# Optimization experiments

Measured on AMD Instinct MI355X. Metric: run time of the kernel, lower is better.

The kernel has to match this reference:

```python
import jax, jax.numpy as jnp
import numpy as np

# dims: N batch, L seq, H heads, d projection_dim, P position_dimension
N, Lq, Lk, H, d, P = 2, 1024, 1024, 8, 64, 1
D = H * d


def _kernel(x):
    # _log_exp_kernel: positive feature map log(1+exp(x)) (softplus)
    return jax.nn.softplus(x)


def setup_inputs() -> dict:
    key = jax.random.key(0)
    ks = jax.random.split(key, 8)
    sc = 1.0 / np.sqrt(D).astype(np.float32)
    return {
        "query": jax.random.normal(ks[0], (N, Lq, D), jnp.float32),
        "key_seq": jax.random.normal(ks[1], (N, Lk, D), jnp.float32),
        "Wq": jax.random.normal(ks[2], (D, D), jnp.float32) * sc,
        "Wk": jax.random.normal(ks[3], (D, D), jnp.float32) * sc,
        "Wv": jax.random.normal(ks[4], (D, D), jnp.float32) * sc,
        "position_coeffs": jax.random.uniform(ks[5], (H, d), jnp.float32, 0.5, 1.5),
        "position_weight": jax.random.normal(ks[6], (H, d, P), jnp.float32) * 1e-3,
        "position_bias": jax.random.normal(ks[7], (H, d), jnp.float32) * 1e-2,
    }


def reference(query, key_seq, Wq, Wk, Wv, position_coeffs, position_weight, position_bias):
    # torch Linear (no bias): y = x @ W.T
    q = _kernel(jnp.einsum('nld,ed->nle', query, Wq).reshape(N, Lq, H, d))
    k = _kernel(jnp.einsum('nld,ed->nle', key_seq, Wk).reshape(N, Lk, H, d))
    v = jnp.einsum('nld,ed->nle', key_seq, Wv).reshape(N, Lk, H, d)
    # (N, H, L, d)
    q = jnp.transpose(q, (0, 2, 1, 3))
    k = jnp.transpose(k, (0, 2, 1, 3))
    v = jnp.transpose(v, (0, 2, 1, 3))

    # default positions: arange, query_offset = 0
    qpos = jnp.broadcast_to(jnp.arange(Lq, dtype=jnp.float32).reshape(1, Lq, 1), (N, Lq, P))
    kpos = jnp.broadcast_to(jnp.arange(Lk, dtype=jnp.float32).reshape(1, Lk, 1), (N, Lk, P))
    pq = jnp.einsum('nlp,hkp->nhlk', qpos, position_weight) + position_bias[None, :, None, :]
    pk = jnp.einsum('nlp,hkp->nhlk', kpos, position_weight)

    coeff = position_coeffs[None, :, None, :]  # (1, H, 1, d)

    def part(f, values):
        # causal (mask_future) linear attention via inclusive cumsum over keys
        Qf = q * f(pq) * coeff           # (N, H, Lq, d)
        Kf = k * f(pk)                   # (N, H, Lk, d)
        S = jnp.cumsum(jnp.einsum('nhkd,nhke->nhkde', Kf, values), axis=2)
        return jnp.einsum('nhqd,nhqde->nhqe', Qf, S)

    num = part(jnp.cos, v) + part(jnp.sin, v)           # (N, H, Lq, d)
    unit = jnp.ones((N, H, Lk, 1), jnp.float32)
    den = part(jnp.cos, unit) + part(jnp.sin, unit)     # (N, H, Lq, 1)
    attn = num / den
    return jnp.transpose(attn, (0, 2, 1, 3)).reshape(N, Lq, D)
```

## Files before the change

kernel.cpp:

```cpp
#include <hip/hip_runtime.h>
#include <cmath>

#define NB    2
#define LSEQ  1024
#define NH    8
#define HD    64
#define DD    512
#define FDIM  128
#define EV    65
#define CHUNK 64
#define NC    16
#define NBH   16

typedef short short8 __attribute__((ext_vector_type(8)));
typedef float floatx4 __attribute__((ext_vector_type(4)));

__device__ __forceinline__ float softplusf(float x) {
  return fmaxf(x, 0.0f) + log1pf(expf(-fabsf(x)));
}

__device__ __forceinline__ unsigned short f2bf(float f) {
  unsigned u = __float_as_uint(f);
  u += 0x7fffu + ((u >> 16) & 1u);
  return (unsigned short)(u >> 16);
}

__device__ __forceinline__ short8 cvt8(float4 a, float4 b) {
  short8 r;
  r[0] = (short)f2bf(a.x); r[1] = (short)f2bf(a.y);
  r[2] = (short)f2bf(a.z); r[3] = (short)f2bf(a.w);
  r[4] = (short)f2bf(b.x); r[5] = (short)f2bf(b.y);
  r[6] = (short)f2bf(b.z); r[7] = (short)f2bf(b.w);
  return r;
}

__global__ __launch_bounds__(256) void k_proj(
    const float* __restrict__ Xq, const float* __restrict__ Xkv,
    const float* __restrict__ Wq, const float* __restrict__ Wk,
    const float* __restrict__ Wv, const float* __restrict__ pw,
    const float* __restrict__ pb, const float* __restrict__ pc,
    float* __restrict__ Qf, float* __restrict__ Kf, float* __restrict__ Vx)
{
  __shared__ short Al[64][72];
  __shared__ short Bl[64][72];
  const int b = blockIdx.x;
  int m0, e0, pmode;
  const float *X, *W;
  if (b < 256) {
    m0 = (b >> 3) << 6; e0 = (b & 7) << 6;
    X = Xq; W = Wq + (size_t)e0 * DD; pmode = 0;
  } else {
    const int bb = b - 256;
    m0 = (bb >> 4) << 6;
    const int nt = bb & 15;
    e0 = (nt & 7) << 6;
    X = Xkv;
    if (nt < 8) { W = Wk + (size_t)e0 * DD; pmode = 1; }
    else        { W = Wv + (size_t)e0 * DD; pmode = 2; }
  }
  const int tid  = threadIdx.x;
  const int r    = tid >> 2;
  const int ko   = (tid & 3) << 4;
  const int wave = tid >> 6, lane = tid & 63;
  const int quad = lane >> 4, lm = lane & 15;
  const float* Ag = X + (size_t)(m0 + r) * DD + ko;
  const float* Bg = W + (size_t)r * DD + ko;
  float4 a[4], bb4[4];
#pragma unroll
  for (int u = 0; u < 4; ++u) {
    a[u]   = *(const float4*)(Ag + (u << 2));
    bb4[u] = *(const float4*)(Bg + (u << 2));
  }
  floatx4 acc[4] = {};
  for (int k0 = 0; k0 < DD; k0 += 64) {
    __syncthreads();
    *(short8*)&Al[r][ko]     = cvt8(a[0], a[1]);
    *(short8*)&Al[r][ko + 8] = cvt8(a[2], a[3]);
    *(short8*)&Bl[r][ko]     = cvt8(bb4[0], bb4[1]);
    *(short8*)&Bl[r][ko + 8] = cvt8(bb4[2], bb4[3]);
    __syncthreads();
    if (k0 + 64 < DD) {
#pragma unroll
      for (int u = 0; u < 4; ++u) {
        a[u]   = *(const float4*)(Ag + k0 + 64 + (u << 2));
        bb4[u] = *(const float4*)(Bg + k0 + 64 + (u << 2));
      }
    }
#pragma unroll
    for (int ks = 0; ks < 2; ++ks) {
      const short8 af = *(const short8*)&Al[(wave << 4) + lm][(quad << 3) + (ks << 5)];
#pragma unroll
      for (int t = 0; t < 4; ++t) {
        const short8 bf = *(const short8*)&Bl[(t << 4) + lm][(quad << 3) + (ks << 5)];
        acc[t] = __builtin_amdgcn_mfma_f32_16x16x32_bf16(af, bf, acc[t], 0, 0, 0);
      }
    }
  }
#pragma unroll
  for (int t = 0; t < 4; ++t) {
    const int e = e0 + (t << 4) + lm;
    const int h = e >> 6, jj = e & 63;
    if (pmode == 2) {
#pragma unroll
      for (int rg = 0; rg < 4; ++rg) {
        const int m = m0 + (wave << 4) + (quad << 2) + rg;
        const int n = m >> 10, l = m & 1023;
        Vx[((size_t)(n * NH + h) * LSEQ + l) * HD + jj] = acc[t][rg];
      }
    } else {
      const float pwv = pw[e];
      const float pbv = (pmode == 0) ? pb[e] : 0.0f;
      const float pcv = (pmode == 0) ? pc[e] : 1.0f;
      float* base = (pmode == 0) ? Qf : Kf;
#pragma unroll
      for (int rg = 0; rg < 4; ++rg) {
        const int m = m0 + (wave << 4) + (quad << 2) + rg;
        const int n = m >> 10, l = m & 1023;
        const float v = softplusf(acc[t][rg]) * pcv;
        const float ang = fmaf((float)l, pwv, pbv);
        const float sn = __sinf(ang), cs = __cosf(ang);
        float* dst = &base[((size_t)(n * NH + h) * LSEQ + l) * FDIM + jj];
        dst[0]  = v * cs;
        dst[64] = v * sn;
      }
    }
  }
}

__global__ __launch_bounds__(256) void k_chunk_sums(
    const float* __restrict__ Kf, const float* __restrict__ Vx,
    float* __restrict__ S)
{
  const int blk = blockIdx.x;
  const int bh  = blk >> 5;
  const int c   = (blk >> 1) & (NC - 1);
  const int fh  = blk & 1;
  const int f0  = fh << 6;
  const int t0  = c * CHUNK;
  const int tid  = threadIdx.x;
  const int wave = tid >> 6, lane = tid & 63;
  const int quad = lane >> 4, lm = lane & 15;

  __shared__ short KT[64][72];
  __shared__ short VT[80][72];

  for (int i = tid; i < 64 * 16; i += 256) {
    const int t = i & 63, f4 = (i >> 6) << 2;
    const float4 k4 = *(const float4*)&Kf[((size_t)bh * LSEQ + t0 + t) * FDIM + f0 + f4];
    KT[f4 + 0][t] = (short)f2bf(k4.x);
    KT[f4 + 1][t] = (short)f2bf(k4.y);
    KT[f4 + 2][t] = (short)f2bf(k4.z);
    KT[f4 + 3][t] = (short)f2bf(k4.w);
  }
  for (int i = tid; i < 64 * 16; i += 256) {
    const int t = i & 63, e4 = (i >> 6) << 2;
    const float4 v4 = *(const float4*)&Vx[((size_t)bh * LSEQ + t0 + t) * HD + e4];
    VT[e4 + 0][t] = (short)f2bf(v4.x);
    VT[e4 + 1][t] = (short)f2bf(v4.y);
    VT[e4 + 2][t] = (short)f2bf(v4.z);
    VT[e4 + 3][t] = (short)f2bf(v4.w);
  }
  if (tid < CHUNK) VT[64][tid] = (short)0x3F80;
  __syncthreads();

  short8 aK[2];
#pragma unroll
  for (int ks = 0; ks < 2; ++ks)
    aK[ks] = *(const short8*)&KT[(wave << 4) + lm][(quad << 3) + (ks << 5)];
  floatx4 acc[5] = {};
#pragma unroll
  for (int nt = 0; nt < 5; ++nt)
#pragma unroll
    for (int ks = 0; ks < 2; ++ks) {
      const short8 bf = *(const short8*)&VT[(nt << 4) + lm][(quad << 3) + (ks << 5)];
      acc[nt] = __builtin_amdgcn_mfma_f32_16x16x32_bf16(aK[ks], bf, acc[nt], 0, 0, 0);
    }

  float* Sb = &S[(size_t)(bh * NC + c) * FDIM * EV];
#pragma unroll
  for (int nt = 0; nt < 4; ++nt)
#pragma unroll
    for (int rg = 0; rg < 4; ++rg) {
      const int f = f0 + (wave << 4) + (quad << 2) + rg;
      Sb[f * EV + (nt << 4) + lm] = acc[nt][rg];
    }
  if (lm == 0) {
#pragma unroll
    for (int rg = 0; rg < 4; ++rg) {
      const int f = f0 + (wave << 4) + (quad << 2) + rg;
      Sb[f * EV + 64] = acc[4][rg];
    }
  }
}

__global__ __launch_bounds__(256) void k_scan(float* __restrict__ S)
{
  const int bh = blockIdx.x >> 4;
  const int fg = blockIdx.x & 15;
  float* Sb = S + (size_t)bh * NC * FDIM * EV + (size_t)fg * 8 * EV;
  const size_t cs = (size_t)FDIM * EV;
  for (int i = threadIdx.x; i < 8 * EV; i += 256) {
    float* p = Sb + i;
    float v[NC];
#pragma unroll
    for (int c = 0; c < NC; ++c) v[c] = p[c * cs];
    float s = 0.0f;
#pragma unroll
    for (int c = 0; c < NC; ++c) { const float t = v[c]; p[c * cs] = s; s += t; }
  }
}

__global__ __launch_bounds__(256) void k_chunk_out(
    const float* __restrict__ Qf, const float* __restrict__ Kf,
    const float* __restrict__ Vx, const float* __restrict__ S,
    float* __restrict__ Out)
{
  const int c  = blockIdx.x & (NC - 1);
  const int bh = blockIdx.x >> 4;
  const int n  = bh >> 3, h = bh & 7;
  const int t0 = c * CHUNK;
  const int tid  = threadIdx.x;
  const int wave = tid >> 6, lane = tid & 63;
  const int quad = lane >> 4, lm = lane & 15;

  __shared__ short QL[64][128];
  __shared__ short KL[64][128];
  __shared__ short ScL[64][72];
  __shared__ short PT[80][136];
  __shared__ short VT[80][72];
  __shared__ float DenL[64];

  const float* Qg = &Qf[((size_t)bh * LSEQ + t0) * FDIM];
  const float* Kg = &Kf[((size_t)bh * LSEQ + t0) * FDIM];
  {
    const int f8 = (tid & 15) << 3;
#pragma unroll
    for (int rr = 0; rr < 64; rr += 16) {
      const int r = rr + (tid >> 4);
      const float4 a0 = *(const float4*)&Qg[r * FDIM + f8];
      const float4 a1 = *(const float4*)&Qg[r * FDIM + f8 + 4];
      *(short8*)&QL[r][f8] = cvt8(a0, a1);
      const float4 b0 = *(const float4*)&Kg[r * FDIM + f8];
      const float4 b1 = *(const float4*)&Kg[r * FDIM + f8 + 4];
      *(short8*)&KL[r][f8] = cvt8(b0, b1);
    }
  }
  {
    const float* Pg = &S[(size_t)(bh * NC + c) * FDIM * EV];
    for (int i = tid; i < FDIM * EV; i += 256) {
      const int f = i / EV, e = i - f * EV;
      PT[e][f] = (short)f2bf(Pg[i]);
    }
  }
  {
    const float* Vg = &Vx[((size_t)bh * LSEQ + t0) * HD];
    for (int i = tid; i < CHUNK * (HD / 4); i += 256) {
      const int t = i >> 4, e4 = (i & 15) << 2;
      const float4 v4 = *(const float4*)&Vg[t * HD + e4];
      VT[e4 + 0][t] = (short)f2bf(v4.x);
      VT[e4 + 1][t] = (short)f2bf(v4.y);
      VT[e4 + 2][t] = (short)f2bf(v4.z);
      VT[e4 + 3][t] = (short)f2bf(v4.w);
    }
    if (tid < CHUNK) VT[64][tid] = (short)0x3F80;
  }
  __syncthreads();

  short8 aQ[4];
#pragma unroll
  for (int ks = 0; ks < 4; ++ks)
    aQ[ks] = *(const short8*)&QL[(wave << 4) + lm][(quad << 3) + (ks << 5)];

  floatx4 accS[4] = {};
#pragma unroll
  for (int nt = 0; nt < 4; ++nt)
#pragma unroll
    for (int ks = 0; ks < 4; ++ks) {
      const short8 b = *(const short8*)&KL[(nt << 4) + lm][(quad << 3) + (ks << 5)];
      accS[nt] = __builtin_amdgcn_mfma_f32_16x16x32_bf16(aQ[ks], b, accS[nt], 0, 0, 0);
    }
#pragma unroll
  for (int nt = 0; nt < 4; ++nt)
#pragma unroll
    for (int rg = 0; rg < 4; ++rg) {
      const int m = (wave << 4) + (quad << 2) + rg;
      const int t = (nt << 4) + lm;
      ScL[m][t] = (short)((t <= m) ? f2bf(accS[nt][rg]) : 0);
    }

  floatx4 accN[5] = {};
#pragma unroll
  for (int nt = 0; nt < 5; ++nt)
#pragma unroll
    for (int ks = 0; ks < 4; ++ks) {
      const short8 b = *(const short8*)&PT[(nt << 4) + lm][(quad << 3) + (ks << 5)];
      accN[nt] = __builtin_amdgcn_mfma_f32_16x16x32_bf16(aQ[ks], b, accN[nt], 0, 0, 0);
    }

  short8 aS[2];
#pragma unroll
  for (int ks = 0; ks < 2; ++ks)
    aS[ks] = *(const short8*)&ScL[(wave << 4) + lm][(quad << 3) + (ks << 5)];
  floatx4 accV[5] = {};
#pragma unroll
  for (int nt = 0; nt < 5; ++nt)
#pragma unroll
    for (int ks = 0; ks < 2; ++ks) {
      const short8 b = *(const short8*)&VT[(nt << 4) + lm][(quad << 3) + (ks << 5)];
      accV[nt] = __builtin_amdgcn_mfma_f32_16x16x32_bf16(aS[ks], b, accV[nt], 0, 0, 0);
    }

  if (lm == 0) {
#pragma unroll
    for (int rg = 0; rg < 4; ++rg)
      DenL[(wave << 4) + (quad << 2) + rg] = accN[4][rg] + accV[4][rg];
  }

#pragma unroll
  for (int rg = 0; rg < 4; ++rg) {
    const int m = (wave << 4) + (quad << 2) + rg;
    const float rden = 1.0f / DenL[m];
    const int l = t0 + m;
#pragma unroll
    for (int nt = 0; nt < 4; ++nt) {
      const float val = (accN[nt][rg] + accV[nt][rg]) * rden;
      Out[((size_t)(n * LSEQ + l)) * DD + h * HD + (nt << 4) + lm] = val;
    }
  }
}

extern "C" void kernel_launch(void* const* d_in, const int* in_sizes, int n_in,
                              void* d_out, int out_size, void* d_ws, size_t ws_size,
                              hipStream_t stream) {
  (void)in_sizes; (void)n_in; (void)out_size; (void)ws_size;
  const float* query  = (const float*)d_in[0];
  const float* keyseq = (const float*)d_in[1];
  const float* Wq     = (const float*)d_in[2];
  const float* Wk     = (const float*)d_in[3];
  const float* Wv     = (const float*)d_in[4];
  const float* pc     = (const float*)d_in[5];
  const float* pw     = (const float*)d_in[6];
  const float* pb     = (const float*)d_in[7];
  float* out = (float*)d_out;

  float* ws = (float*)d_ws;
  float* Qf = ws;
  float* Kf = Qf + (size_t)NBH * LSEQ * FDIM;
  float* Vx = Kf + (size_t)NBH * LSEQ * FDIM;
  float* S  = Vx + (size_t)NBH * LSEQ * HD;

  k_proj      <<<768,          256, 0, stream>>>(query, keyseq, Wq, Wk, Wv, pw, pb, pc, Qf, Kf, Vx);
  k_chunk_sums<<<NBH * NC * 2, 256, 0, stream>>>(Kf, Vx, S);
  k_scan      <<<NBH * NC,     256, 0, stream>>>(S);
  k_chunk_out <<<NBH * NC,     256, 0, stream>>>(Qf, Kf, Vx, S, out);
}
```

Baseline: 119.4 us.

## Store intermediates as bf16 in MFMA-ready layouts and read fragments directly

```diff
diff --git a/kernel.cpp b/kernel.cpp
--- a/kernel.cpp
+++ b/kernel.cpp
@@ -14,15 +14,16 @@
 
 typedef short short8 __attribute__((ext_vector_type(8)));
 typedef float floatx4 __attribute__((ext_vector_type(4)));
+typedef unsigned short ushort;
 
 __device__ __forceinline__ float softplusf(float x) {
   return fmaxf(x, 0.0f) + log1pf(expf(-fabsf(x)));
 }
 
-__device__ __forceinline__ unsigned short f2bf(float f) {
+__device__ __forceinline__ ushort f2bf(float f) {
   unsigned u = __float_as_uint(f);
   u += 0x7fffu + ((u >> 16) & 1u);
-  return (unsigned short)(u >> 16);
+  return (ushort)(u >> 16);
 }
 
 __device__ __forceinline__ short8 cvt8(float4 a, float4 b) {
@@ -39,7 +40,8 @@
     const float* __restrict__ Wq, const float* __restrict__ Wk,
     const float* __restrict__ Wv, const float* __restrict__ pw,
     const float* __restrict__ pb, const float* __restrict__ pc,
-    float* __restrict__ Qf, float* __restrict__ Kf, float* __restrict__ Vx)
+    ushort* __restrict__ Qfb, ushort* __restrict__ Kfb,
+    ushort* __restrict__ VTb)
 {
   __shared__ short Al[64][72];
   __shared__ short Bl[64][72];
@@ -96,39 +98,46 @@
       }
     }
   }
-#pragma unroll
-  for (int t = 0; t < 4; ++t) {
-    const int e = e0 + (t << 4) + lm;
-    const int h = e >> 6, jj = e & 63;
-    if (pmode == 2) {
+  if (pmode == 2) {
+    const int h  = e0 >> 6;
+    const int n  = m0 >> 10;
+    const int l0 = m0 & 1023;
+    const int bh = n * NH + h;
+#pragma unroll
+    for (int t = 0; t < 4; ++t) {
+      const int jj = (t << 4) + lm;
 #pragma unroll
       for (int rg = 0; rg < 4; ++rg) {
-        const int m = m0 + (wave << 4) + (quad << 2) + rg;
-        const int n = m >> 10, l = m & 1023;
-        Vx[((size_t)(n * NH + h) * LSEQ + l) * HD + jj] = acc[t][rg];
+        const int l = l0 + (wave << 4) + (quad << 2) + rg;
+        VTb[((size_t)bh * 80 + jj) * LSEQ + l] = f2bf(acc[t][rg]);
       }
-    } else {
+    }
+    if (tid < 64) VTb[((size_t)bh * 80 + 64) * LSEQ + l0 + tid] = 0x3F80u;
+  } else {
+    ushort* base = (pmode == 0) ? Qfb : Kfb;
+#pragma unroll
+    for (int t = 0; t < 4; ++t) {
+      const int e = e0 + (t << 4) + lm;
+      const int h = e >> 6, jj = e & 63;
       const float pwv = pw[e];
       const float pbv = (pmode == 0) ? pb[e] : 0.0f;
       const float pcv = (pmode == 0) ? pc[e] : 1.0f;
-      float* base = (pmode == 0) ? Qf : Kf;
 #pragma unroll
       for (int rg = 0; rg < 4; ++rg) {
         const int m = m0 + (wave << 4) + (quad << 2) + rg;
         const int n = m >> 10, l = m & 1023;
         const float v = softplusf(acc[t][rg]) * pcv;
         const float ang = fmaf((float)l, pwv, pbv);
-        const float sn = __sinf(ang), cs = __cosf(ang);
-        float* dst = &base[((size_t)(n * NH + h) * LSEQ + l) * FDIM + jj];
-        dst[0]  = v * cs;
-        dst[64] = v * sn;
+        ushort* dst = &base[((size_t)(n * NH + h) * LSEQ + l) * FDIM + jj];
+        dst[0]  = f2bf(v * __cosf(ang));
+        dst[64] = f2bf(v * __sinf(ang));
       }
     }
   }
 }
 
 __global__ __launch_bounds__(256) void k_chunk_sums(
-    const float* __restrict__ Kf, const float* __restrict__ Vx,
+    const ushort* __restrict__ Kfb, const ushort* __restrict__ VTb,
     float* __restrict__ S)
 {
   const int blk = blockIdx.x;
@@ -142,25 +151,13 @@
   const int quad = lane >> 4, lm = lane & 15;
 
   __shared__ short KT[64][72];
-  __shared__ short VT[80][72];
-
-  for (int i = tid; i < 64 * 16; i += 256) {
-    const int t = i & 63, f4 = (i >> 6) << 2;
-    const float4 k4 = *(const float4*)&Kf[((size_t)bh * LSEQ + t0 + t) * FDIM + f0 + f4];
-    KT[f4 + 0][t] = (short)f2bf(k4.x);
-    KT[f4 + 1][t] = (short)f2bf(k4.y);
-    KT[f4 + 2][t] = (short)f2bf(k4.z);
-    KT[f4 + 3][t] = (short)f2bf(k4.w);
-  }
-  for (int i = tid; i < 64 * 16; i += 256) {
-    const int t = i & 63, e4 = (i >> 6) << 2;
-    const float4 v4 = *(const float4*)&Vx[((size_t)bh * LSEQ + t0 + t) * HD + e4];
-    VT[e4 + 0][t] = (short)f2bf(v4.x);
-    VT[e4 + 1][t] = (short)f2bf(v4.y);
-    VT[e4 + 2][t] = (short)f2bf(v4.z);
-    VT[e4 + 3][t] = (short)f2bf(v4.w);
-  }
-  if (tid < CHUNK) VT[64][tid] = (short)0x3F80;
+
+  for (int i = tid; i < 64 * 8; i += 256) {
+    const int t = i & 63, f8 = (i >> 6) << 3;
+    const short8 k8 = *(const short8*)&Kfb[((size_t)bh * LSEQ + t0 + t) * FDIM + f0 + f8];
+#pragma unroll
+    for (int u = 0; u < 8; ++u) KT[f8 + u][t] = k8[u];
+  }
   __syncthreads();
 
   short8 aK[2];
@@ -172,7 +169,8 @@
   for (int nt = 0; nt < 5; ++nt)
 #pragma unroll
     for (int ks = 0; ks < 2; ++ks) {
-      const short8 bf = *(const short8*)&VT[(nt << 4) + lm][(quad << 3) + (ks << 5)];
+      const short8 bf = *(const short8*)
+          &VTb[((size_t)bh * 80 + (nt << 4) + lm) * LSEQ + t0 + (quad << 3) + (ks << 5)];
       acc[nt] = __builtin_amdgcn_mfma_f32_16x16x32_bf16(aK[ks], bf, acc[nt], 0, 0, 0);
     }
 
@@ -193,26 +191,31 @@
   }
 }
 
-__global__ __launch_bounds__(256) void k_scan(float* __restrict__ S)
+__global__ __launch_bounds__(256) void k_scan(
+    const float* __restrict__ S, ushort* __restrict__ PTb)
 {
-  const int bh = blockIdx.x >> 4;
-  const int fg = blockIdx.x & 15;
-  float* Sb = S + (size_t)bh * NC * FDIM * EV + (size_t)fg * 8 * EV;
+  const int bh = blockIdx.x / 13;
+  const int eg = blockIdx.x % 13;
   const size_t cs = (size_t)FDIM * EV;
-  for (int i = threadIdx.x; i < 8 * EV; i += 256) {
-    float* p = Sb + i;
+  for (int i = threadIdx.x; i < 5 * FDIM; i += 256) {
+    const int e = eg * 5 + (i >> 7);
+    const int f = i & 127;
+    const float* p = S + (size_t)(bh * NC) * cs + f * EV + e;
     float v[NC];
 #pragma unroll
     for (int c = 0; c < NC; ++c) v[c] = p[c * cs];
     float s = 0.0f;
 #pragma unroll
-    for (int c = 0; c < NC; ++c) { const float t = v[c]; p[c * cs] = s; s += t; }
+    for (int c = 0; c < NC; ++c) {
+      PTb[((size_t)(bh * NC + c) * 80 + e) * 128 + f] = f2bf(s);
+      s += v[c];
+    }
   }
 }
 
 __global__ __launch_bounds__(256) void k_chunk_out(
-    const float* __restrict__ Qf, const float* __restrict__ Kf,
-    const float* __restrict__ Vx, const float* __restrict__ S,
+    const ushort* __restrict__ Qfb, const ushort* __restrict__ Kfb,
+    const ushort* __restrict__ VTb, const ushort* __restrict__ PTb,
     float* __restrict__ Out)
 {
   const int c  = blockIdx.x & (NC - 1);
@@ -223,60 +226,23 @@
   const int wave = tid >> 6, lane = tid & 63;
   const int quad = lane >> 4, lm = lane & 15;
 
-  __shared__ short QL[64][128];
-  __shared__ short KL[64][128];
   __shared__ short ScL[64][72];
-  __shared__ short PT[80][136];
-  __shared__ short VT[80][72];
   __shared__ float DenL[64];
 
-  const float* Qg = &Qf[((size_t)bh * LSEQ + t0) * FDIM];
-  const float* Kg = &Kf[((size_t)bh * LSEQ + t0) * FDIM];
-  {
-    const int f8 = (tid & 15) << 3;
-#pragma unroll
-    for (int rr = 0; rr < 64; rr += 16) {
-      const int r = rr + (tid >> 4);
-      const float4 a0 = *(const float4*)&Qg[r * FDIM + f8];
-      const float4 a1 = *(const float4*)&Qg[r * FDIM + f8 + 4];
-      *(short8*)&QL[r][f8] = cvt8(a0, a1);
-      const float4 b0 = *(const float4*)&Kg[r * FDIM + f8];
-      const float4 b1 = *(const float4*)&Kg[r * FDIM + f8 + 4];
-      *(short8*)&KL[r][f8] = cvt8(b0, b1);
-    }
-  }
-  {
-    const float* Pg = &S[(size_t)(bh * NC + c) * FDIM * EV];
-    for (int i = tid; i < FDIM * EV; i += 256) {
-      const int f = i / EV, e = i - f * EV;
-      PT[e][f] = (short)f2bf(Pg[i]);
-    }
-  }
-  {
-    const float* Vg = &Vx[((size_t)bh * LSEQ + t0) * HD];
-    for (int i = tid; i < CHUNK * (HD / 4); i += 256) {
-      const int t = i >> 4, e4 = (i & 15) << 2;
-      const float4 v4 = *(const float4*)&Vg[t * HD + e4];
-      VT[e4 + 0][t] = (short)f2bf(v4.x);
-      VT[e4 + 1][t] = (short)f2bf(v4.y);
-      VT[e4 + 2][t] = (short)f2bf(v4.z);
-      VT[e4 + 3][t] = (short)f2bf(v4.w);
-    }
-    if (tid < CHUNK) VT[64][tid] = (short)0x3F80;
-  }
-  __syncthreads();
+  const size_t qkBase = (size_t)bh * LSEQ + t0;
+  const int ks_off = quad << 3;
 
   short8 aQ[4];
 #pragma unroll
   for (int ks = 0; ks < 4; ++ks)
-    aQ[ks] = *(const short8*)&QL[(wave << 4) + lm][(quad << 3) + (ks << 5)];
+    aQ[ks] = *(const short8*)&Qfb[(qkBase + (wave << 4) + lm) * FDIM + ks_off + (ks << 5)];
 
   floatx4 accS[4] = {};
 #pragma unroll
   for (int nt = 0; nt < 4; ++nt)
 #pragma unroll
     for (int ks = 0; ks < 4; ++ks) {
-      const short8 b = *(const short8*)&KL[(nt << 4) + lm][(quad << 3) + (ks << 5)];
+      const short8 b = *(const short8*)&Kfb[(qkBase + (nt << 4) + lm) * FDIM + ks_off + (ks << 5)];
       accS[nt] = __builtin_amdgcn_mfma_f32_16x16x32_bf16(aQ[ks], b, accS[nt], 0, 0, 0);
     }
 #pragma unroll
@@ -288,25 +254,27 @@
       ScL[m][t] = (short)((t <= m) ? f2bf(accS[nt][rg]) : 0);
     }
 
+  const ushort* Pg = &PTb[(size_t)(bh * NC + c) * 80 * 128];
   floatx4 accN[5] = {};
 #pragma unroll
   for (int nt = 0; nt < 5; ++nt)
 #pragma unroll
     for (int ks = 0; ks < 4; ++ks) {
-      const short8 b = *(const short8*)&PT[(nt << 4) + lm][(quad << 3) + (ks << 5)];
+      const short8 b = *(const short8*)&Pg[(size_t)((nt << 4) + lm) * 128 + ks_off + (ks << 5)];
       accN[nt] = __builtin_amdgcn_mfma_f32_16x16x32_bf16(aQ[ks], b, accN[nt], 0, 0, 0);
     }
 
   short8 aS[2];
 #pragma unroll
   for (int ks = 0; ks < 2; ++ks)
-    aS[ks] = *(const short8*)&ScL[(wave << 4) + lm][(quad << 3) + (ks << 5)];
+    aS[ks] = *(const short8*)&ScL[(wave << 4) + lm][ks_off + (ks << 5)];
   floatx4 accV[5] = {};
 #pragma unroll
   for (int nt = 0; nt < 5; ++nt)
 #pragma unroll
     for (int ks = 0; ks < 2; ++ks) {
-      const short8 b = *(const short8*)&VT[(nt << 4) + lm][(quad << 3) + (ks << 5)];
+      const short8 b = *(const short8*)
+          &VTb[((size_t)bh * 80 + (nt << 4) + lm) * LSEQ + t0 + ks_off + (ks << 5)];
       accV[nt] = __builtin_amdgcn_mfma_f32_16x16x32_bf16(aS[ks], b, accV[nt], 0, 0, 0);
     }
 
@@ -343,14 +311,14 @@
   const float* pb     = (const float*)d_in[7];
   float* out = (float*)d_out;
 
-  float* ws = (float*)d_ws;
-  float* Qf = ws;
-  float* Kf = Qf + (size_t)NBH * LSEQ * FDIM;
-  float* Vx = Kf + (size_t)NBH * LSEQ * FDIM;
-  float* S  = Vx + (size_t)NBH * LSEQ * HD;
-
-  k_proj      <<<768,          256, 0, stream>>>(query, keyseq, Wq, Wk, Wv, pw, pb, pc, Qf, Kf, Vx);
-  k_chunk_sums<<<NBH * NC * 2, 256, 0, stream>>>(Kf, Vx, S);
-  k_scan      <<<NBH * NC,     256, 0, stream>>>(S);
-  k_chunk_out <<<NBH * NC,     256, 0, stream>>>(Qf, Kf, Vx, S, out);
-}
+  ushort* Qfb = (ushort*)d_ws;
+  ushort* Kfb = Qfb + (size_t)NBH * LSEQ * FDIM;
+  ushort* VTb = Kfb + (size_t)NBH * LSEQ * FDIM;
+  float*  S   = (float*)(VTb + (size_t)NBH * 80 * LSEQ);
+  ushort* PTb = (ushort*)(S + (size_t)NBH * NC * FDIM * EV);
+
+  k_proj      <<<768,          256, 0, stream>>>(query, keyseq, Wq, Wk, Wv, pw, pb, pc, Qfb, Kfb, VTb);
+  k_chunk_sums<<<NBH * NC * 2, 256, 0, stream>>>(Kfb, VTb, S);
+  k_scan      <<<NBH * 13,     256, 0, stream>>>(S, PTb);
+  k_chunk_out <<<NBH * NC,     256, 0, stream>>>(Qfb, Kfb, VTb, PTb, out);
+}
```

Result: slower. 131.5 us (+10.1%).

## Fuse chunk prefix scan into output kernel and transpose chunk-sum layout

Applied to the files above, without the earlier changes.

```diff
diff --git a/kernel.cpp b/kernel.cpp
--- a/kernel.cpp
+++ b/kernel.cpp
@@ -8,6 +8,7 @@
 #define DD    512
 #define FDIM  128
 #define EV    65
+#define SEP   80
 #define CHUNK 64
 #define NC    16
 #define NBH   16
@@ -176,37 +177,20 @@
       acc[nt] = __builtin_amdgcn_mfma_f32_16x16x32_bf16(aK[ks], bf, acc[nt], 0, 0, 0);
     }
 
-  float* Sb = &S[(size_t)(bh * NC + c) * FDIM * EV];
+  float* Sb = &S[(size_t)(bh * NC + c) * SEP * FDIM];
 #pragma unroll
   for (int nt = 0; nt < 4; ++nt)
 #pragma unroll
     for (int rg = 0; rg < 4; ++rg) {
       const int f = f0 + (wave << 4) + (quad << 2) + rg;
-      Sb[f * EV + (nt << 4) + lm] = acc[nt][rg];
+      Sb[((nt << 4) + lm) * FDIM + f] = acc[nt][rg];
     }
   if (lm == 0) {
 #pragma unroll
     for (int rg = 0; rg < 4; ++rg) {
       const int f = f0 + (wave << 4) + (quad << 2) + rg;
-      Sb[f * EV + 64] = acc[4][rg];
-    }
-  }
-}
-
-__global__ __launch_bounds__(256) void k_scan(float* __restrict__ S)
-{
-  const int bh = blockIdx.x >> 4;
-  const int fg = blockIdx.x & 15;
-  float* Sb = S + (size_t)bh * NC * FDIM * EV + (size_t)fg * 8 * EV;
-  const size_t cs = (size_t)FDIM * EV;
-  for (int i = threadIdx.x; i < 8 * EV; i += 256) {
-    float* p = Sb + i;
-    float v[NC];
-#pragma unroll
-    for (int c = 0; c < NC; ++c) v[c] = p[c * cs];
-    float s = 0.0f;
-#pragma unroll
-    for (int c = 0; c < NC; ++c) { const float t = v[c]; p[c * cs] = s; s += t; }
+      Sb[64 * FDIM + f] = acc[4][rg];
+    }
   }
 }
 
@@ -246,10 +230,19 @@
     }
   }
   {
-    const float* Pg = &S[(size_t)(bh * NC + c) * FDIM * EV];
-    for (int i = tid; i < FDIM * EV; i += 256) {
-      const int f = i / EV, e = i - f * EV;
-      PT[e][f] = (short)f2bf(Pg[i]);
+    const float* Sg = &S[(size_t)(bh * NC) * SEP * FDIM];
+    for (int i0 = tid; i0 < SEP * FDIM; i0 += 256 * 8) {
+      float s[8] = {};
+      for (int cc = 0; cc < c; ++cc) {
+        const float* p = Sg + (size_t)cc * SEP * FDIM + i0;
+#pragma unroll
+        for (int u = 0; u < 8; ++u) s[u] += p[u * 256];
+      }
+#pragma unroll
+      for (int u = 0; u < 8; ++u) {
+        const int i = i0 + u * 256;
+        PT[i >> 7][i & 127] = (short)f2bf(s[u]);
+      }
     }
   }
   {
@@ -351,6 +344,5 @@
 
   k_proj      <<<768,          256, 0, stream>>>(query, keyseq, Wq, Wk, Wv, pw, pb, pc, Qf, Kf, Vx);
   k_chunk_sums<<<NBH * NC * 2, 256, 0, stream>>>(Kf, Vx, S);
-  k_scan      <<<NBH * NC,     256, 0, stream>>>(S);
   k_chunk_out <<<NBH * NC,     256, 0, stream>>>(Qf, Kf, Vx, S, out);
 }
```

Result: slower. 129.9 us (+8.8%).
